# Performance work log

Hardware: AMD Instinct MI355X
Metric: run time of the kernel (lower is better)

Reference implementation:

```python
import jax, jax.numpy as jnp
import numpy as np
import math

B, N, D, H = 2, 96, 64, 4  # batch, num_nodes, d_model, num_heads
DK = D // H


def setup_inputs() -> dict:
    key = jax.random.key(0)
    ks = jax.random.split(key, 11)
    s = 0.02
    return {
        "state": jax.random.normal(ks[0], (B, N * N, D), jnp.float32),
        "w_lk": jax.random.normal(ks[1], (D, D), jnp.float32) * s,
        "b_lk": jax.random.normal(ks[2], (D,), jnp.float32) * s,
        "w_rk": jax.random.normal(ks[3], (D, D), jnp.float32) * s,
        "b_rk": jax.random.normal(ks[4], (D,), jnp.float32) * s,
        "w_lv": jax.random.normal(ks[5], (D, D), jnp.float32) * s,
        "b_lv": jax.random.normal(ks[6], (D,), jnp.float32) * s,
        "w_rv": jax.random.normal(ks[7], (D, D), jnp.float32) * s,
        "b_rv": jax.random.normal(ks[8], (D,), jnp.float32) * s,
        "w_out": jax.random.normal(ks[9], (D, D), jnp.float32) * s,
        "b_out": jax.random.normal(ks[10], (D,), jnp.float32) * s,
    }


def reference(state, w_lk, b_lk, w_rk, b_rk, w_lv, b_lv, w_rv, b_rv, w_out, b_out):
    b = state.shape[0]
    n = int(np.sqrt(state.shape[1]))
    d_model = state.shape[2]
    h, dk = H, d_model // H

    def lin(x, w, bias):  # torch nn.Linear: x @ W^T + b
        return x @ w.T + bias

    # project and view as [b, n, n, h, dk]
    lk = lin(state, w_lk, b_lk).reshape(b, n, n, h, dk)
    rk = lin(state, w_rk, b_rk).reshape(b, n, n, h, dk)
    lv = lin(state, w_lv, b_lv).reshape(b, n, n, h, dk)
    rv = lin(state, w_rv, b_rv).reshape(b, n, n, h, dk)

    # triangular edge-attention scores over intermediate node a
    scores = jnp.einsum('bxahd,bayhd->bxayh', lk, rk) / math.sqrt(dk)
    att = jax.nn.softmax(scores, axis=2)  # softmax over a

    # fused contraction: equivalent to val = lv[x,a]*rv[a,y] then sum_a att*val,
    # without materializing the O(n^3 * d) val tensor
    x = jnp.einsum('bxayh,bxahd,bayhd->bxyhd', att, lv, rv)

    x = x.reshape(b, n * n, d_model)
    return lin(x, w_out, b_out)
```

## Files before the change

kernel.cpp:

```cpp
#include <hip/hip_runtime.h>

#define NB     96
#define ELEM_B 589824
#define TENS   1179648
#define T_ROWS 18432

__device__ __forceinline__ void proj_tile(
    const float* __restrict__ src, const float* __restrict__ w,
    const float* __restrict__ bias, float* __restrict__ dst,
    int row0, int t, float* sw, float* srow, float* sb)
{
#pragma unroll
    for (int j = 0; j < 4; ++j) {
        const int s = t + j * 256;
        const int c = s >> 4, k4 = s & 15;
        *(float4*)&sw[c * 68 + k4 * 4] = *(const float4*)(w + s * 4);
    }
#pragma unroll
    for (int j = 0; j < 2; ++j) {
        const int s = t + j * 256;
        *(float4*)&srow[s * 4] = *(const float4*)(src + row0 * 64 + s * 4);
    }
    if (t < 64) sb[t] = bias[t];
    __syncthreads();

    const int c = t & 63, rg = t >> 6;
    float acc[8];
#pragma unroll
    for (int r = 0; r < 8; ++r) acc[r] = sb[c];
#pragma unroll
    for (int k4 = 0; k4 < 16; ++k4) {
        const float4 w4 = *(const float4*)&sw[c * 68 + k4 * 4];
#pragma unroll
        for (int r = 0; r < 8; ++r) {
            const float4 s4 = *(const float4*)&srow[(rg * 8 + r) * 64 + k4 * 4];
            acc[r] = fmaf(s4.x, w4.x, acc[r]);
            acc[r] = fmaf(s4.y, w4.y, acc[r]);
            acc[r] = fmaf(s4.z, w4.z, acc[r]);
            acc[r] = fmaf(s4.w, w4.w, acc[r]);
        }
    }
#pragma unroll
    for (int r = 0; r < 8; ++r)
        dst[(row0 + rg * 8 + r) * 64 + c] = acc[r];
}

__global__ __launch_bounds__(256) void proj4_kernel(
    const float* __restrict__ state,
    const float* __restrict__ w0, const float* __restrict__ b0,
    const float* __restrict__ w1, const float* __restrict__ b1,
    const float* __restrict__ w2, const float* __restrict__ b2,
    const float* __restrict__ w3, const float* __restrict__ b3,
    float* __restrict__ o0, float* __restrict__ o1,
    float* __restrict__ o2, float* __restrict__ o3)
{
    __shared__ float sw[64 * 68];
    __shared__ float srow[32 * 64];
    __shared__ float sb[64];
    const int mat  = blockIdx.x & 3;
    const int row0 = (blockIdx.x >> 2) * 32;
    const float* w = (mat == 0) ? w0 : (mat == 1) ? w1 : (mat == 2) ? w2 : w3;
    const float* b = (mat == 0) ? b0 : (mat == 1) ? b1 : (mat == 2) ? b2 : b3;
    float* o       = (mat == 0) ? o0 : (mat == 1) ? o1 : (mat == 2) ? o2 : o3;
    proj_tile(state, w, b, o, row0, threadIdx.x, sw, srow, sb);
}

__global__ __launch_bounds__(256) void proj1_kernel(
    const float* __restrict__ src, const float* __restrict__ w,
    const float* __restrict__ b, float* __restrict__ dst)
{
    __shared__ float sw[64 * 68];
    __shared__ float srow[32 * 64];
    __shared__ float sb[64];
    proj_tile(src, w, b, dst, blockIdx.x * 32, threadIdx.x, sw, srow, sb);
}

__global__ __launch_bounds__(384) void scores_kernel(
    const float* __restrict__ lk, const float* __restrict__ rk,
    float* __restrict__ P)
{
    __shared__ float lks[96][16];
    const int bid = blockIdx.x;
    const int a  = bid % 96;
    const int bh = bid / 96;
    const int b  = bh >> 2, h = bh & 3;
    const int t  = threadIdx.x;
    const int base = b * ELEM_B + h * 16;

    {
        const int row = t >> 2, q = t & 3;
        *(float4*)&lks[row][q * 4] =
            *(const float4*)(lk + base + (row * 96 + a) * 64 + q * 4);
    }
    const int y = t % 96, xg = t / 96;
    const float4* rkp = (const float4*)(rk + base + (a * 96 + y) * 64);
    const float4 r0 = rkp[0], r1 = rkp[1], r2 = rkp[2], r3 = rkp[3];
    __syncthreads();

    float* Pout = P + (size_t)(bh * 96) * 9216 + a * 96 + y;
#pragma unroll 4
    for (int i = 0; i < 24; ++i) {
        const int x = xg * 24 + i;
        const float4* lp = (const float4*)lks[x];
        const float4 l0 = lp[0], l1 = lp[1], l2 = lp[2], l3 = lp[3];
        float s = l0.x * r0.x;
        s = fmaf(l0.y, r0.y, s); s = fmaf(l0.z, r0.z, s); s = fmaf(l0.w, r0.w, s);
        s = fmaf(l1.x, r1.x, s); s = fmaf(l1.y, r1.y, s); s = fmaf(l1.z, r1.z, s);
        s = fmaf(l1.w, r1.w, s); s = fmaf(l2.x, r2.x, s); s = fmaf(l2.y, r2.y, s);
        s = fmaf(l2.z, r2.z, s); s = fmaf(l2.w, r2.w, s); s = fmaf(l3.x, r3.x, s);
        s = fmaf(l3.y, r3.y, s); s = fmaf(l3.z, r3.z, s); s = fmaf(l3.w, r3.w, s);
        Pout[(size_t)x * 9216] = __expf(s * 0.25f);
    }
}

__global__ __launch_bounds__(384) void contract_kernel(
    const float* __restrict__ lv, const float* __restrict__ rv,
    const float* __restrict__ P, float* __restrict__ xb)
{
    __shared__ float lvs[6][96][16];
    __shared__ float rvs[4][48][16];
    __shared__ float Ps[6][4][48];
    const int bid = blockIdx.x;
    const int xt = bid & 15, yh = (bid >> 4) & 1, bh = bid >> 5;
    const int b = bh >> 2, h = bh & 3;
    const int x0 = xt * 6, y0 = yh * 48;
    const int t = threadIdx.x;
    const int base = b * ELEM_B + h * 16;
    const size_t pbase = (size_t)(bh * 96) * 9216;

#pragma unroll
    for (int j = 0; j < 6; ++j) {
        const int s = t + j * 384;
        const int xi = s / 384, rem = s % 384, aa = rem >> 2, q = rem & 3;
        *(float4*)&lvs[xi][aa][q * 4] =
            *(const float4*)(lv + base + ((x0 + xi) * 96 + aa) * 64 + q * 4);
    }

    const int dq = t & 3, q2 = t >> 2;
    const int y = q2 % 48, xg = q2 / 48;

    float4 acc[3]; float den[3];
#pragma unroll
    for (int xl = 0; xl < 3; ++xl) {
        acc[xl] = make_float4(0.f, 0.f, 0.f, 0.f);
        den[xl] = 0.f;
    }

    float4 rpre[2]; float ppre[3];
#pragma unroll
    for (int j = 0; j < 2; ++j) {
        const int s = t + j * 384;
        const int ai = s / 192, rem = s % 192, yy = rem >> 2, qq = rem & 3;
        rpre[j] = *(const float4*)(rv + base + ((ai) * 96 + y0 + yy) * 64 + qq * 4);
    }
#pragma unroll
    for (int j = 0; j < 3; ++j) {
        const int s = t + j * 384;
        const int xi = s / 192, rem = s % 192, ai = rem / 48, yy = rem % 48;
        ppre[j] = P[pbase + (size_t)(x0 + xi) * 9216 + ai * 96 + y0 + yy];
    }

    for (int at = 0; at < 24; ++at) {
        __syncthreads();
#pragma unroll
        for (int j = 0; j < 2; ++j) {
            const int s = t + j * 384;
            *(float4*)&((float*)rvs)[s * 4] = rpre[j];
        }
#pragma unroll
        for (int j = 0; j < 3; ++j) {
            const int s = t + j * 384;
            ((float*)Ps)[s] = ppre[j];
        }
        __syncthreads();
        if (at < 23) {
            const int a0n = (at + 1) * 4;
#pragma unroll
            for (int j = 0; j < 2; ++j) {
                const int s = t + j * 384;
                const int ai = s / 192, rem = s % 192, yy = rem >> 2, qq = rem & 3;
                rpre[j] = *(const float4*)(rv + base + ((a0n + ai) * 96 + y0 + yy) * 64 + qq * 4);
            }
#pragma unroll
            for (int j = 0; j < 3; ++j) {
                const int s = t + j * 384;
                const int xi = s / 192, rem = s % 192, ai = rem / 48, yy = rem % 48;
                ppre[j] = P[pbase + (size_t)(x0 + xi) * 9216 + (a0n + ai) * 96 + y0 + yy];
            }
        }
        const int abase = at * 4;
#pragma unroll
        for (int ai = 0; ai < 4; ++ai) {
            const float4 r4 = *(const float4*)&rvs[ai][y][dq * 4];
#pragma unroll
            for (int xl = 0; xl < 3; ++xl) {
                const int xi = xg * 3 + xl;
                const float p = Ps[xi][ai][y];
                const float4 l4 = *(const float4*)&lvs[xi][abase + ai][dq * 4];
                den[xl] += p;
                acc[xl].x = fmaf(p * l4.x, r4.x, acc[xl].x);
                acc[xl].y = fmaf(p * l4.y, r4.y, acc[xl].y);
                acc[xl].z = fmaf(p * l4.z, r4.z, acc[xl].z);
                acc[xl].w = fmaf(p * l4.w, r4.w, acc[xl].w);
            }
        }
    }

#pragma unroll
    for (int xl = 0; xl < 3; ++xl) {
        const int xi = xg * 3 + xl;
        const float inv = 1.0f / den[xl];
        float4 o;
        o.x = acc[xl].x * inv; o.y = acc[xl].y * inv;
        o.z = acc[xl].z * inv; o.w = acc[xl].w * inv;
        *(float4*)(xb + base + ((x0 + xi) * 96 + y0 + y) * 64 + dq * 4) = o;
    }
}

extern "C" void kernel_launch(void* const* d_in, const int* in_sizes, int n_in,
                              void* d_out, int out_size, void* d_ws, size_t ws_size,
                              hipStream_t stream)
{
    const float* state = (const float*)d_in[0];
    const float* w_lk  = (const float*)d_in[1];
    const float* b_lk  = (const float*)d_in[2];
    const float* w_rk  = (const float*)d_in[3];
    const float* b_rk  = (const float*)d_in[4];
    const float* w_lv  = (const float*)d_in[5];
    const float* b_lv  = (const float*)d_in[6];
    const float* w_rv  = (const float*)d_in[7];
    const float* b_rv  = (const float*)d_in[8];
    const float* w_out = (const float*)d_in[9];
    const float* b_out = (const float*)d_in[10];
    float* out = (float*)d_out;

    float* ws = (float*)d_ws;
    float* lk = ws;
    float* rk = ws + (size_t)TENS;
    float* lv = ws + (size_t)2 * TENS;
    float* rv = ws + (size_t)3 * TENS;
    float* xb = ws + (size_t)4 * TENS;
    float* P  = ws + (size_t)5 * TENS;

    proj4_kernel<<<4 * (T_ROWS / 32), 256, 0, stream>>>(
        state, w_lk, b_lk, w_rk, b_rk, w_lv, b_lv, w_rv, b_rv, lk, rk, lv, rv);
    scores_kernel<<<8 * 96, 384, 0, stream>>>(lk, rk, P);
    contract_kernel<<<256, 384, 0, stream>>>(lv, rv, P, xb);
    proj1_kernel<<<T_ROWS / 32, 256, 0, stream>>>(xb, w_out, b_out, out);
}
```

Baseline: 147.6 us.

## Retile contraction for more blocks, stream rv/P directly, double projection rows per block

The contraction kernel is restructured from 256 blocks that each stage rv and P tiles through shared memory with double-buffered prefetch into 768 smaller blocks. Each thread now computes one output and reads rv and P straight from global memory inside an unrolled loop over a, with only lv kept in shared memory. The goal is more parallelism across the GPU's compute units and no per-iteration barriers. In exchange, reuse of rv and P across x rows is lost, which raises global and cache traffic. Separately, the projection kernels process 64 rows per block instead of 32, halving the grid size and giving each thread more accumulators per loaded weight.

```diff
diff --git a/kernel.cpp b/kernel.cpp
--- a/kernel.cpp
+++ b/kernel.cpp
@@ -1,11 +1,10 @@
 #include <hip/hip_runtime.h>
 
-#define NB     96
 #define ELEM_B 589824
 #define TENS   1179648
 #define T_ROWS 18432
 
-__device__ __forceinline__ void proj_tile(
+__device__ __forceinline__ void proj_tile64(
     const float* __restrict__ src, const float* __restrict__ w,
     const float* __restrict__ bias, float* __restrict__ dst,
     int row0, int t, float* sw, float* srow, float* sb)
@@ -17,7 +16,7 @@
         *(float4*)&sw[c * 68 + k4 * 4] = *(const float4*)(w + s * 4);
     }
 #pragma unroll
-    for (int j = 0; j < 2; ++j) {
+    for (int j = 0; j < 4; ++j) {
         const int s = t + j * 256;
         *(float4*)&srow[s * 4] = *(const float4*)(src + row0 * 64 + s * 4);
     }
@@ -25,15 +24,15 @@
     __syncthreads();
 
     const int c = t & 63, rg = t >> 6;
-    float acc[8];
+    float acc[16];
 #pragma unroll
-    for (int r = 0; r < 8; ++r) acc[r] = sb[c];
+    for (int r = 0; r < 16; ++r) acc[r] = sb[c];
 #pragma unroll
     for (int k4 = 0; k4 < 16; ++k4) {
         const float4 w4 = *(const float4*)&sw[c * 68 + k4 * 4];
 #pragma unroll
-        for (int r = 0; r < 8; ++r) {
-            const float4 s4 = *(const float4*)&srow[(rg * 8 + r) * 64 + k4 * 4];
+        for (int r = 0; r < 16; ++r) {
+            const float4 s4 = *(const float4*)&srow[(rg * 16 + r) * 64 + k4 * 4];
             acc[r] = fmaf(s4.x, w4.x, acc[r]);
             acc[r] = fmaf(s4.y, w4.y, acc[r]);
             acc[r] = fmaf(s4.z, w4.z, acc[r]);
@@ -41,8 +40,8 @@
         }
     }
 #pragma unroll
-    for (int r = 0; r < 8; ++r)
-        dst[(row0 + rg * 8 + r) * 64 + c] = acc[r];
+    for (int r = 0; r < 16; ++r)
+        dst[(row0 + rg * 16 + r) * 64 + c] = acc[r];
 }
 
 __global__ __launch_bounds__(256) void proj4_kernel(
@@ -55,14 +54,14 @@
     float* __restrict__ o2, float* __restrict__ o3)
 {
     __shared__ float sw[64 * 68];
-    __shared__ float srow[32 * 64];
+    __shared__ float srow[64 * 64];
     __shared__ float sb[64];
     const int mat  = blockIdx.x & 3;
-    const int row0 = (blockIdx.x >> 2) * 32;
+    const int row0 = (blockIdx.x >> 2) * 64;
     const float* w = (mat == 0) ? w0 : (mat == 1) ? w1 : (mat == 2) ? w2 : w3;
     const float* b = (mat == 0) ? b0 : (mat == 1) ? b1 : (mat == 2) ? b2 : b3;
     float* o       = (mat == 0) ? o0 : (mat == 1) ? o1 : (mat == 2) ? o2 : o3;
-    proj_tile(state, w, b, o, row0, threadIdx.x, sw, srow, sb);
+    proj_tile64(state, w, b, o, row0, threadIdx.x, sw, srow, sb);
 }
 
 __global__ __launch_bounds__(256) void proj1_kernel(
@@ -70,9 +69,9 @@
     const float* __restrict__ b, float* __restrict__ dst)
 {
     __shared__ float sw[64 * 68];
-    __shared__ float srow[32 * 64];
+    __shared__ float srow[64 * 64];
     __shared__ float sb[64];
-    proj_tile(src, w, b, dst, blockIdx.x * 32, threadIdx.x, sw, srow, sb);
+    proj_tile64(src, w, b, dst, blockIdx.x * 64, threadIdx.x, sw, srow, sb);
 }
 
 __global__ __launch_bounds__(384) void scores_kernel(
@@ -117,104 +116,52 @@
     const float* __restrict__ lv, const float* __restrict__ rv,
     const float* __restrict__ P, float* __restrict__ xb)
 {
-    __shared__ float lvs[6][96][16];
-    __shared__ float rvs[4][48][16];
-    __shared__ float Ps[6][4][48];
+    __shared__ float lvs[4][96][16];
     const int bid = blockIdx.x;
-    const int xt = bid & 15, yh = (bid >> 4) & 1, bh = bid >> 5;
+    const int yq = bid & 3;
+    const int xt = (bid >> 2) % 24;
+    const int bh = bid / 96;
     const int b = bh >> 2, h = bh & 3;
-    const int x0 = xt * 6, y0 = yh * 48;
+    const int x0 = xt * 4, y0 = yq * 24;
     const int t = threadIdx.x;
     const int base = b * ELEM_B + h * 16;
-    const size_t pbase = (size_t)(bh * 96) * 9216;
 
+    {
+        const int aa = t >> 2, q = t & 3;
 #pragma unroll
-    for (int j = 0; j < 6; ++j) {
-        const int s = t + j * 384;
-        const int xi = s / 384, rem = s % 384, aa = rem >> 2, q = rem & 3;
-        *(float4*)&lvs[xi][aa][q * 4] =
-            *(const float4*)(lv + base + ((x0 + xi) * 96 + aa) * 64 + q * 4);
+        for (int j = 0; j < 4; ++j)
+            *(float4*)&lvs[j][aa][q * 4] =
+                *(const float4*)(lv + base + ((x0 + j) * 96 + aa) * 64 + q * 4);
+    }
+    __syncthreads();
+
+    const int dq = t & 3;
+    const int q2 = t >> 2;
+    const int y  = q2 % 24;
+    const int xi = q2 / 24;
+    const int yy = y0 + y;
+
+    const float* rvp = rv + base + yy * 64 + dq * 4;
+    const float* Pp  = P + (size_t)(bh * 96) * 9216 + (size_t)(x0 + xi) * 9216 + yy;
+
+    float4 acc = make_float4(0.f, 0.f, 0.f, 0.f);
+    float den = 0.f;
+#pragma unroll 8
+    for (int a = 0; a < 96; ++a) {
+        const float4 r4 = *(const float4*)(rvp + a * 6144);
+        const float  p  = Pp[a * 96];
+        const float4 l4 = *(const float4*)&lvs[xi][a][dq * 4];
+        den += p;
+        acc.x = fmaf(p * l4.x, r4.x, acc.x);
+        acc.y = fmaf(p * l4.y, r4.y, acc.y);
+        acc.z = fmaf(p * l4.z, r4.z, acc.z);
+        acc.w = fmaf(p * l4.w, r4.w, acc.w);
     }
 
-    const int dq = t & 3, q2 = t >> 2;
-    const int y = q2 % 48, xg = q2 / 48;
-
-    float4 acc[3]; float den[3];
-#pragma unroll
-    for (int xl = 0; xl < 3; ++xl) {
-        acc[xl] = make_float4(0.f, 0.f, 0.f, 0.f);
-        den[xl] = 0.f;
-    }
-
-    float4 rpre[2]; float ppre[3];
-#pragma unroll
-    for (int j = 0; j < 2; ++j) {
-        const int s = t + j * 384;
-        const int ai = s / 192, rem = s % 192, yy = rem >> 2, qq = rem & 3;
-        rpre[j] = *(const float4*)(rv + base + ((ai) * 96 + y0 + yy) * 64 + qq * 4);
-    }
-#pragma unroll
-    for (int j = 0; j < 3; ++j) {
-        const int s = t + j * 384;
-        const int xi = s / 192, rem = s % 192, ai = rem / 48, yy = rem % 48;
-        ppre[j] = P[pbase + (size_t)(x0 + xi) * 9216 + ai * 96 + y0 + yy];
-    }
-
-    for (int at = 0; at < 24; ++at) {
-        __syncthreads();
-#pragma unroll
-        for (int j = 0; j < 2; ++j) {
-            const int s = t + j * 384;
-            *(float4*)&((float*)rvs)[s * 4] = rpre[j];
-        }
-#pragma unroll
-        for (int j = 0; j < 3; ++j) {
-            const int s = t + j * 384;
-            ((float*)Ps)[s] = ppre[j];
-        }
-        __syncthreads();
-        if (at < 23) {
-            const int a0n = (at + 1) * 4;
-#pragma unroll
-            for (int j = 0; j < 2; ++j) {
-                const int s = t + j * 384;
-                const int ai = s / 192, rem = s % 192, yy = rem >> 2, qq = rem & 3;
-                rpre[j] = *(const float4*)(rv + base + ((a0n + ai) * 96 + y0 + yy) * 64 + qq * 4);
-            }
-#pragma unroll
-            for (int j = 0; j < 3; ++j) {
-                const int s = t + j * 384;
-                const int xi = s / 192, rem = s % 192, ai = rem / 48, yy = rem % 48;
-                ppre[j] = P[pbase + (size_t)(x0 + xi) * 9216 + (a0n + ai) * 96 + y0 + yy];
-            }
-        }
-        const int abase = at * 4;
-#pragma unroll
-        for (int ai = 0; ai < 4; ++ai) {
-            const float4 r4 = *(const float4*)&rvs[ai][y][dq * 4];
-#pragma unroll
-            for (int xl = 0; xl < 3; ++xl) {
-                const int xi = xg * 3 + xl;
-                const float p = Ps[xi][ai][y];
-                const float4 l4 = *(const float4*)&lvs[xi][abase + ai][dq * 4];
-                den[xl] += p;
-                acc[xl].x = fmaf(p * l4.x, r4.x, acc[xl].x);
-                acc[xl].y = fmaf(p * l4.y, r4.y, acc[xl].y);
-                acc[xl].z = fmaf(p * l4.z, r4.z, acc[xl].z);
-                acc[xl].w = fmaf(p * l4.w, r4.w, acc[xl].w);
-            }
-        }
-    }
-
-#pragma unroll
-    for (int xl = 0; xl < 3; ++xl) {
-        const int xi = xg * 3 + xl;
-        const float inv = 1.0f / den[xl];
-        float4 o;
-        o.x = acc[xl].x * inv; o.y = acc[xl].y * inv;
-        o.z = acc[xl].z * inv; o.w = acc[xl].w * inv;
-        *(float4*)(xb + base + ((x0 + xi) * 96 + y0 + y) * 64 + dq * 4) = o;
-    }
+    const float inv = 1.0f / den;
+    float4 o;
+    o.x = acc.x * inv; o.y = acc.y * inv; o.z = acc.z * inv; o.w = acc.w * inv;
+    *(float4*)(xb + base + ((x0 + xi) * 96 + yy) * 64 + dq * 4) = o;
 }
 
 extern "C" void kernel_launch(void* const* d_in, const int* in_sizes, int n_in,
@@ -242,9 +189,9 @@
     float* xb = ws + (size_t)4 * TENS;
     float* P  = ws + (size_t)5 * TENS;
 
-    proj4_kernel<<<4 * (T_ROWS / 32), 256, 0, stream>>>(
+    proj4_kernel<<<4 * (T_ROWS / 64), 256, 0, stream>>>(
         state, w_lk, b_lk, w_rk, b_rk, w_lv, b_lv, w_rv, b_rv, lk, rk, lv, rv);
     scores_kernel<<<8 * 96, 384, 0, stream>>>(lk, rk, P);
-    contract_kernel<<<256, 384, 0, stream>>>(lv, rv, P, xb);
-    proj1_kernel<<<T_ROWS / 32, 256, 0, stream>>>(xb, w_out, b_out, out);
+    contract_kernel<<<768, 384, 0, stream>>>(lv, rv, P, xb);
+    proj1_kernel<<<T_ROWS / 64, 256, 0, stream>>>(xb, w_out, b_out, out);
 }
```

Result: slower. 156.9 us (+6.3%).
